# Optimization experiments

Hardware: AMD Instinct MI355X
Metric: run time of the kernel (lower is better)

## Reference

```python
import jax, jax.numpy as jnp
import numpy as np

K = 3          # kernel size
PAD = 1        # (K-1)//2, stride=1, dilation=1


def _modulated_deform_conv(depth, offset, mask, w, b):
    """torchvision deform_conv2d with in_ch=out_ch=1, stride=1, pad=1, dil=1.
    depth:  [B,1,H,W]
    offset: [B,2*K*K,H,W]  interleaved (dy, dx) per kernel tap
    mask:   [B,K*K,H,W]    modulation scalars
    w:      [1,1,K,K]      conv weights (ones buffer)
    b:      [1]            bias (zeros buffer)
    """
    B, _, H, W = depth.shape
    kk = K * K
    img = depth[:, 0]                                    # [B,H,W]

    off = offset.reshape(B, kk, 2, H, W)
    dy, dx = off[:, :, 0], off[:, :, 1]                  # [B,kk,H,W]

    # integer tap offsets of the 3x3 kernel
    ky, kx = jnp.meshgrid(jnp.arange(K), jnp.arange(K), indexing='ij')
    ky = ky.reshape(kk).astype(depth.dtype)
    kx = kx.reshape(kk).astype(depth.dtype)

    iy = jnp.arange(H, dtype=depth.dtype)
    ix = jnp.arange(W, dtype=depth.dtype)
    # sampling coords per output pixel per tap: [B,kk,H,W]
    y = iy[None, None, :, None] - PAD + ky[None, :, None, None] + dy
    x = ix[None, None, None, :] - PAD + kx[None, :, None, None] + dx

    y0f = jnp.floor(y); x0f = jnp.floor(x)
    wy = y - y0f; wx = x - x0f                           # frac parts
    y0 = y0f.astype(jnp.int32); x0 = x0f.astype(jnp.int32)
    y1 = y0 + 1;  x1 = x0 + 1

    bidx = jnp.arange(B)[:, None, None, None]

    def corner(yc, xc):
        inb = (yc >= 0) & (yc < H) & (xc >= 0) & (xc < W)
        v = img[bidx, jnp.clip(yc, 0, H - 1), jnp.clip(xc, 0, W - 1)]
        return jnp.where(inb, v, jnp.zeros((), depth.dtype))

    sampled = (corner(y0, x0) * (1 - wy) * (1 - wx)
             + corner(y0, x1) * (1 - wy) * wx
             + corner(y1, x0) * wy * (1 - wx)
             + corner(y1, x1) * wy * wx)                 # [B,kk,H,W]

    wk = w.reshape(1, kk, 1, 1)
    out = jnp.sum(sampled * mask * wk, axis=1) + b[0]    # [B,H,W]
    return out[:, None]                                  # [B,1,H,W]


def setup_inputs() -> dict:
    key = jax.random.key(0)
    k1, k2, k3 = jax.random.split(key, 3)
    B, H, W = 8, 512, 512
    depth  = jax.random.normal(k1, (B, 1, H, W), dtype=jnp.float32)
    weight = jax.random.uniform(k2, (B, K * K, H, W), dtype=jnp.float32)
    offset = jax.random.normal(k3, (B, 2 * K * K, H, W), dtype=jnp.float32)
    w = jnp.ones((1, 1, K, K), dtype=jnp.float32)   # buffer 'w'
    b = jnp.zeros((1,), dtype=jnp.float32)          # buffer 'b'
    return {"depth": depth, "weight": weight, "offset": offset, "w": w, "b": b}


def reference(depth, weight, offset, w, b):
    return _modulated_deform_conv(depth, offset, weight, w, b)
```

## Files before the change

kernel.cpp:

```cpp
#include <hip/hip_runtime.h>


#define KK 9
#define PAD 1
#define H 512
#define W 512
#define HW (H * W)

#define TX 64
#define TY 8
#define HALO 8
#define LW (TX + 2 * HALO)
#define LH (TY + 2 * HALO)

typedef float f2 __attribute__((ext_vector_type(2)));

__device__ __forceinline__ float bilin_global(const float* __restrict__ img,
                                              float y, float x) {
    float y0f = floorf(y);
    float x0f = floorf(x);
    int y0 = (int)y0f;
    int x0 = (int)x0f;
    float wy = y - y0f;
    float wx = x - x0f;
    int y1 = y0 + 1;
    int x1 = x0 + 1;

    bool y0i = (y0 >= 0) & (y0 < H);
    bool y1i = (y1 >= 0) & (y1 < H);
    bool x0i = (x0 >= 0) & (x0 < W);
    bool x1i = (x1 >= 0) & (x1 < W);

    int y0c = min(max(y0, 0), H - 1);
    int y1c = min(max(y1, 0), H - 1);
    int x0c = min(max(x0, 0), W - 1);
    int x1c = min(max(x1, 0), W - 1);

    float v00 = (y0i & x0i) ? img[y0c * W + x0c] : 0.0f;
    float v01 = (y0i & x1i) ? img[y0c * W + x1c] : 0.0f;
    float v10 = (y1i & x0i) ? img[y1c * W + x0c] : 0.0f;
    float v11 = (y1i & x1i) ? img[y1c * W + x1c] : 0.0f;

    float omwy = 1.0f - wy;
    float omwx = 1.0f - wx;
    return fmaf(v00 * omwy, omwx,
           fmaf(v01 * omwy, wx,
           fmaf(v10 * wy,   omwx, v11 * wy * wx)));
}

__device__ __forceinline__ float sample_tile(const float* __restrict__ S,
                                             const float* __restrict__ img,
                                             int tY0, int tX0,
                                             float sy, float sx) {
    const float y0f = floorf(sy);
    const float x0f = floorf(sx);
    const float wy = sy - y0f;
    const float wx = sx - x0f;
    const int ly0 = (int)y0f - tY0;
    const int lx0 = (int)x0f - tX0;

    if (((unsigned)ly0 < (unsigned)(LH - 1)) &
        ((unsigned)lx0 < (unsigned)(LW - 1))) {
        const int s = ly0 * LW + lx0;
        const float v00 = S[s];
        const float v01 = S[s + 1];
        const float v10 = S[s + LW];
        const float v11 = S[s + LW + 1];
        const float omwy = 1.0f - wy;
        const float omwx = 1.0f - wx;
        return fmaf(v00 * omwy, omwx,
               fmaf(v01 * omwy, wx,
               fmaf(v10 * wy,   omwx, v11 * wy * wx)));
    }
    return bilin_global(img, sy, sx);
}

__global__ void dcn_kernel(
    const float* __restrict__ depth,
    const float* __restrict__ mask,
    const float* __restrict__ offset,
    const float* __restrict__ w9,
    const float* __restrict__ bias,
    float* __restrict__ out) {
    __shared__ float S[LH * LW];

    const int b  = blockIdx.z;
    const int bx = blockIdx.x;
    const int by = blockIdx.y;
    const int tX0 = bx * TX - HALO;
    const int tY0 = by * TY - HALO;

    const float* __restrict__ img = depth + (long)b * HW;

    for (int i = threadIdx.x; i < LH * LW; i += 256) {
        const int ly = i / LW;
        const int lx = i - ly * LW;
        const int gy = tY0 + ly;
        const int gx = tX0 + lx;
        float v = 0.0f;
        if (((unsigned)gy < (unsigned)H) & ((unsigned)gx < (unsigned)W))
            v = img[gy * W + gx];
        S[i] = v;
    }
    __syncthreads();

    const int xp = threadIdx.x & 31;
    const int yr = threadIdx.x >> 5;
    const int tx = bx * TX + 2 * xp;
    const int ty = by * TY + yr;
    const int pix = ty * W + tx;

    const float* __restrict__ msk = mask   + ((long)b * KK)     * HW + pix;
    const float* __restrict__ off = offset + ((long)b * 2 * KK) * HW + pix;

    f2 dyv[KK], dxv[KK], mv[KK];
    #pragma unroll
    for (int k = 0; k < KK; ++k) {
        dyv[k] = *(const f2*)(off + (2 * k) * HW);
        dxv[k] = *(const f2*)(off + (2 * k + 1) * HW);
        mv[k]  = *(const f2*)(msk + k * HW);
    }

    __builtin_amdgcn_sched_barrier(0);

    const float bs = bias[0];
    float a0 = bs, a1 = bs;
    const float syb = (float)(ty - PAD);
    const float sxb = (float)(tx - PAD);

    #pragma unroll
    for (int k = 0; k < KK; ++k) {
        const int ky = k / 3;
        const int kx = k - ky * 3;
        const float wk = w9[k];
        const float sy = syb + (float)ky;
        const float sx = sxb + (float)kx;

        a0 = fmaf(sample_tile(S, img, tY0, tX0, sy + dyv[k].x, sx + 0.0f + dxv[k].x),
                  mv[k].x * wk, a0);
        a1 = fmaf(sample_tile(S, img, tY0, tX0, sy + dyv[k].y, sx + 1.0f + dxv[k].y),
                  mv[k].y * wk, a1);
    }

    f2 r; r.x = a0; r.y = a1;
    *(f2*)(out + (long)b * HW + pix) = r;
}

extern "C" void kernel_launch(void* const* d_in, const int* in_sizes, int n_in,
                              void* d_out, int out_size, void* d_ws, size_t ws_size,
                              hipStream_t stream) {
    const float* depth  = (const float*)d_in[0];
    const float* mask   = (const float*)d_in[1];
    const float* offset = (const float*)d_in[2];
    const float* w9     = (const float*)d_in[3];
    const float* bias   = (const float*)d_in[4];
    float* out = (float*)d_out;

    const int B = in_sizes[0] / HW;

    dim3 block(256);
    dim3 grid(W / TX, H / TY, B);
    dcn_kernel<<<grid, block, 0, stream>>>(depth, mask, offset, w9, bias, out);
}
```

Before: 270.3 us.

## Branchless LDS sampling with clamped index and deferred per-thread global fallback

Replaces the per-tap branch between the LDS tile and global memory with branchless LDS sampling. The LDS index is clamped to a safe range and any out-of-tile access sets a per-thread flag, and only flagged threads redo all taps from global memory at the end. It also pads the LDS row stride by one to reduce bank conflicts, issues the offset and mask loads before the tile fill so they overlap it, and sets launch bounds for occupancy. The cost is redundant recomputation for threads whose offsets fall outside the halo.

```diff
diff --git a/kernel.cpp b/kernel.cpp
--- a/kernel.cpp
+++ b/kernel.cpp
@@ -10,8 +10,10 @@
 #define TX 64
 #define TY 8
 #define HALO 8
-#define LW (TX + 2 * HALO)
-#define LH (TY + 2 * HALO)
+#define LWL (TX + 2 * HALO)
+#define LH  (TY + 2 * HALO)
+#define LWS (LWL + 1)
+#define SAFE ((LH - 2) * LWS + (LWL - 2))
 
 typedef float f2 __attribute__((ext_vector_type(2)));
 
@@ -48,41 +50,37 @@
            fmaf(v10 * wy,   omwx, v11 * wy * wx)));
 }
 
-__device__ __forceinline__ float sample_tile(const float* __restrict__ S,
-                                             const float* __restrict__ img,
-                                             int tY0, int tX0,
-                                             float sy, float sx) {
-    const float y0f = floorf(sy);
-    const float x0f = floorf(sx);
-    const float wy = sy - y0f;
-    const float wx = sx - x0f;
-    const int ly0 = (int)y0f - tY0;
-    const int lx0 = (int)x0f - tX0;
-
-    if (((unsigned)ly0 < (unsigned)(LH - 1)) &
-        ((unsigned)lx0 < (unsigned)(LW - 1))) {
-        const int s = ly0 * LW + lx0;
-        const float v00 = S[s];
-        const float v01 = S[s + 1];
-        const float v10 = S[s + LW];
-        const float v11 = S[s + LW + 1];
-        const float omwy = 1.0f - wy;
-        const float omwx = 1.0f - wx;
-        return fmaf(v00 * omwy, omwx,
-               fmaf(v01 * omwy, wx,
-               fmaf(v10 * wy,   omwx, v11 * wy * wx)));
-    }
-    return bilin_global(img, sy, sx);
+__device__ __forceinline__ float sample_nb(const float* S, float syr, float sxr,
+                                           int& oob) {
+    const float y0f = floorf(syr);
+    const float x0f = floorf(sxr);
+    const float wy = syr - y0f;
+    const float wx = sxr - x0f;
+    const int ly = (int)y0f;
+    const int lx = (int)x0f;
+    oob |= (int)(((unsigned)ly >= (unsigned)(LH - 1)) |
+                 ((unsigned)lx >= (unsigned)(LWL - 1)));
+    unsigned su = (unsigned)(ly * LWS + lx);
+    su = su < (unsigned)SAFE ? su : (unsigned)SAFE;
+    const float v00 = S[su];
+    const float v01 = S[su + 1];
+    const float v10 = S[su + LWS];
+    const float v11 = S[su + LWS + 1];
+    const float omwy = 1.0f - wy;
+    const float omwx = 1.0f - wx;
+    return fmaf(v00 * omwy, omwx,
+           fmaf(v01 * omwy, wx,
+           fmaf(v10 * wy,   omwx, v11 * wy * wx)));
 }
 
-__global__ void dcn_kernel(
+__global__ __launch_bounds__(256, 5) void dcn_kernel(
     const float* __restrict__ depth,
     const float* __restrict__ mask,
     const float* __restrict__ offset,
     const float* __restrict__ w9,
     const float* __restrict__ bias,
     float* __restrict__ out) {
-    __shared__ float S[LH * LW];
+    __shared__ float S[LH * LWS];
 
     const int b  = blockIdx.z;
     const int bx = blockIdx.x;
@@ -91,18 +89,6 @@
     const int tY0 = by * TY - HALO;
 
     const float* __restrict__ img = depth + (long)b * HW;
-
-    for (int i = threadIdx.x; i < LH * LW; i += 256) {
-        const int ly = i / LW;
-        const int lx = i - ly * LW;
-        const int gy = tY0 + ly;
-        const int gx = tX0 + lx;
-        float v = 0.0f;
-        if (((unsigned)gy < (unsigned)H) & ((unsigned)gx < (unsigned)W))
-            v = img[gy * W + gx];
-        S[i] = v;
-    }
-    __syncthreads();
 
     const int xp = threadIdx.x & 31;
     const int yr = threadIdx.x >> 5;
@@ -113,36 +99,78 @@
     const float* __restrict__ msk = mask   + ((long)b * KK)     * HW + pix;
     const float* __restrict__ off = offset + ((long)b * 2 * KK) * HW + pix;
 
-    f2 dyv[KK], dxv[KK], mv[KK];
-    #pragma unroll
-    for (int k = 0; k < KK; ++k) {
-        dyv[k] = *(const f2*)(off + (2 * k) * HW);
-        dxv[k] = *(const f2*)(off + (2 * k + 1) * HW);
-        mv[k]  = *(const f2*)(msk + k * HW);
+    f2 dy0, dy1, dy2, dy3, dy4, dy5, dy6, dy7, dy8;
+    f2 dx0, dx1, dx2, dx3, dx4, dx5, dx6, dx7, dx8;
+    f2 m0, m1, m2, m3, m4, m5, m6, m7, m8;
+#define LDT(k)                                              \
+    dy##k = *(const f2*)(off + (2 * k) * HW);               \
+    dx##k = *(const f2*)(off + (2 * k + 1) * HW);           \
+    m##k  = *(const f2*)(msk + k * HW);
+    LDT(0) LDT(1) LDT(2) LDT(3) LDT(4) LDT(5) LDT(6) LDT(7) LDT(8)
+#undef LDT
+    __builtin_amdgcn_sched_barrier(0);
+
+    for (int i = threadIdx.x; i < LH * LWL; i += 256) {
+        const int ly = i / LWL;
+        const int lx = i - ly * LWL;
+        const int gy = tY0 + ly;
+        const int gx = tX0 + lx;
+        float v = 0.0f;
+        if (((unsigned)gy < (unsigned)H) & ((unsigned)gx < (unsigned)W))
+            v = img[gy * W + gx];
+        S[ly * LWS + lx] = v;
     }
-
-    __builtin_amdgcn_sched_barrier(0);
+    __syncthreads();
 
     const float bs = bias[0];
     float a0 = bs, a1 = bs;
-    const float syb = (float)(ty - PAD);
-    const float sxb = (float)(tx - PAD);
+    int oob = 0;
+    const float sybr = (float)(yr + HALO - PAD);
+    const float sxbr = (float)(2 * xp + HALO - PAD);
 
-    #pragma unroll
-    for (int k = 0; k < KK; ++k) {
-        const int ky = k / 3;
-        const int kx = k - ky * 3;
-        const float wk = w9[k];
-        const float sy = syb + (float)ky;
-        const float sx = sxb + (float)kx;
+#define CTAP(k, KYC, KXC)                                                     \
+    {                                                                         \
+        const float wk = w9[k];                                               \
+        const float syA = sybr + (float)(KYC) + dy##k.x;                      \
+        const float sxA = sxbr + (float)(KXC) + dx##k.x;                      \
+        a0 = fmaf(sample_nb(S, syA, sxA, oob), m##k.x * wk, a0);              \
+        const float syB = sybr + (float)(KYC) + dy##k.y;                      \
+        const float sxB = sxbr + (float)(KXC) + 1.0f + dx##k.y;               \
+        a1 = fmaf(sample_nb(S, syB, sxB, oob), m##k.y * wk, a1);              \
+    }
+    CTAP(0, 0, 0) CTAP(1, 0, 1) CTAP(2, 0, 2)
+    CTAP(3, 1, 0) CTAP(4, 1, 1) CTAP(5, 1, 2)
+    CTAP(6, 2, 0) CTAP(7, 2, 1) CTAP(8, 2, 2)
+#undef CTAP
 
-        a0 = fmaf(sample_tile(S, img, tY0, tX0, sy + dyv[k].x, sx + 0.0f + dxv[k].x),
-                  mv[k].x * wk, a0);
-        a1 = fmaf(sample_tile(S, img, tY0, tX0, sy + dyv[k].y, sx + 1.0f + dxv[k].y),
-                  mv[k].y * wk, a1);
+    if (__builtin_expect(__any(oob), 0)) {
+        if (oob) {
+            a0 = bs;
+            a1 = bs;
+#pragma unroll 1
+            for (int k = 0; k < KK; ++k) {
+                const int ky = k / 3;
+                const int kx = k - 3 * ky;
+                const float wk = w9[k];
+                const float fdy0 = off[(2 * k) * HW];
+                const float fdy1 = off[(2 * k) * HW + 1];
+                const float fdx0 = off[(2 * k + 1) * HW];
+                const float fdx1 = off[(2 * k + 1) * HW + 1];
+                const float fm0 = msk[k * HW];
+                const float fm1 = msk[k * HW + 1];
+                const float syA = (float)(ty - PAD + ky) + fdy0;
+                const float sxA = (float)(tx - PAD + kx) + fdx0;
+                a0 = fmaf(bilin_global(img, syA, sxA), fm0 * wk, a0);
+                const float syB = (float)(ty - PAD + ky) + fdy1;
+                const float sxB = (float)(tx - PAD + kx + 1) + fdx1;
+                a1 = fmaf(bilin_global(img, syB, sxB), fm1 * wk, a1);
+            }
+        }
     }
 
-    f2 r; r.x = a0; r.y = a1;
+    f2 r;
+    r.x = a0;
+    r.y = a1;
     *(f2*)(out + (long)b * HW + pix) = r;
 }
 
```

Result: no change. 274.5 us (+1.6%).
